# Kernel tuning notes

Measured on AMD Instinct MI355X. Metric: run time of the kernel, lower is better.

## Reference

```python
import jax, jax.numpy as jnp
import numpy as np

NUM_SAMPLE = 80  # hardcoded in the original forward
NUM_ACT = 6
NUM_OPP = 3


def setup_inputs() -> dict:
    key = jax.random.key(0)
    k0, k1, k2 = jax.random.split(key, 3)
    B, D = 4096, 512
    x = jax.random.normal(k0, (B, D), dtype=jnp.float32)
    # orthogonal init with gain 0.01 -> small weights; approximate scale
    W_opp = jax.random.normal(k1, (NUM_OPP, D, NUM_ACT), dtype=jnp.float32) * 0.01
    b_opp = jnp.zeros((NUM_OPP, NUM_ACT), dtype=jnp.float32)
    W = jax.random.normal(k2, (D + NUM_OPP * NUM_ACT, NUM_ACT), dtype=jnp.float32) * 0.01
    b = jnp.zeros((NUM_ACT,), dtype=jnp.float32)
    return {"x": x, "W_opp": W_opp, "b_opp": b_opp, "W": W, "b": b}


def reference(x, W_opp, b_opp, W, b):
    B, D = x.shape
    # --- opponent actors: small linear + softmax, vectorized over the 3 opponents ---
    logits = jnp.einsum('bd,kda->kba', x, W_opp) + b_opp[:, None, :]   # [3,B,6]
    dist = jax.nn.softmax(logits, axis=-1)                              # [3,B,6]
    logp = jax.nn.log_softmax(logits, axis=-1)
    # entropy.mean() per opponent, then sum/3 == mean over opponents
    entropy = (-(dist * logp).sum(-1)).mean(-1).mean()

    # --- vectorized categorical sampling: 80 samples per opponent per batch elem ---
    skey = jax.random.key(42)
    samples = jax.random.categorical(skey, logits[:, None], axis=-1,
                                     shape=(NUM_OPP, NUM_SAMPLE, B))   # [3,S,B] int

    # gather sampled-action probabilities
    probs = jnp.take_along_axis(dist[:, None], samples[..., None], axis=-1)[..., 0]  # [3,S,B]
    probs_bt = jnp.transpose(probs, (0, 2, 1))                          # [3,B,S]
    p1 = probs_bt[0] * probs_bt[1] * probs_bt[2]                        # [B,S]
    p2 = p1 / p1.sum(axis=1, keepdims=True)                             # normalized joint weights

    # actions3[b,s,k] = sampled action of opponent k, sample s, batch b
    acts = jnp.transpose(samples, (2, 1, 0))                            # [B,S,3]
    oh = jax.nn.one_hot(acts, NUM_ACT, dtype=x.dtype).reshape(B, NUM_SAMPLE, NUM_OPP * NUM_ACT)  # [B,S,18]

    xa = jnp.broadcast_to(x[:, None, :], (B, NUM_SAMPLE, D))            # replicate x per sample
    a = jnp.concatenate([xa, oh], axis=2)                               # [B,S,D+18]
    agent_probs = jax.nn.softmax(a @ W + b, axis=-1)                    # [B,S,6]

    actions_probs = jnp.einsum('bs,bsa->ba', p2, agent_probs)           # [B,6]
    return actions_probs, dist, entropy
```

## Files before the change

kernel.cpp:

```cpp
#include <hip/hip_runtime.h>
#include <stdint.h>

#define NUM_ACT 6
#define NUM_OPP 3
#define NUM_SAMPLE 80
#define BATCH 4096
#define DIM 512
#define ACC_STRIDE 98304
#define TROWS 32
#define ENT_IDX 98304

__device__ __forceinline__ uint32_t rotl32(uint32_t x, int d) {
  return (x << d) | (x >> (32 - d));
}

__device__ __forceinline__ void tf_round4(uint32_t& x0, uint32_t& x1,
                                          int r0, int r1, int r2, int r3) {
  x0 += x1; x1 = rotl32(x1, r0); x1 ^= x0;
  x0 += x1; x1 = rotl32(x1, r1); x1 ^= x0;
  x0 += x1; x1 = rotl32(x1, r2); x1 ^= x0;
  x0 += x1; x1 = rotl32(x1, r3); x1 ^= x0;
}

__device__ __forceinline__ void threefry2x32(uint32_t k0, uint32_t k1,
                                             uint32_t& x0, uint32_t& x1) {
  const uint32_t ks2 = k0 ^ k1 ^ 0x1BD11BDAu;
  x0 += k0;  x1 += k1;
  tf_round4(x0, x1, 13, 15, 26, 6);  x0 += k1;  x1 += ks2 + 1u;
  tf_round4(x0, x1, 17, 29, 16, 24); x0 += ks2; x1 += k0  + 2u;
  tf_round4(x0, x1, 13, 15, 26, 6);  x0 += k0;  x1 += k1  + 3u;
  tf_round4(x0, x1, 17, 29, 16, 24); x0 += k1;  x1 += ks2 + 4u;
  tf_round4(x0, x1, 13, 15, 26, 6);  x0 += ks2; x1 += k0  + 5u;
}

__device__ __forceinline__ float jax_uniform(uint32_t flat_idx) {
  uint32_t x0 = 0u, x1 = flat_idx;
  threefry2x32(0u, 42u, x0, x1);
  uint32_t bits = x0 ^ x1;
  return __uint_as_float((bits >> 9) | 0x3f800000u) - 1.0f;
}

__device__ __forceinline__ void dot4(float& a, float4 u, float4 v) {
  a = fmaf(u.x, v.x, a); a = fmaf(u.y, v.y, a);
  a = fmaf(u.z, v.z, a); a = fmaf(u.w, v.w, a);
}

template<int NCH>
__global__ __launch_bounds__(128) void k1_gemm(
    const float* __restrict__ x, const float* __restrict__ Wopp,
    const float* __restrict__ W, float* __restrict__ part,
    float* __restrict__ out) {
  constexpr int WIDTH = 512 / NCH;
  constexpr int XSTR = WIDTH + 4;
  const int tile = blockIdx.x / NCH;
  const int ch = blockIdx.x % NCH;
  const int rowbase = tile * TROWS;
  const int dbase = ch * WIDTH;
  __shared__ float xs[TROWS * XSTR];
  __shared__ float wt[24 * XSTR];
  const int t = threadIdx.x;

  for (int f = t; f < TROWS * (WIDTH / 4); f += 128) {
    int row = f / (WIDTH / 4), c4 = (f % (WIDTH / 4)) << 2;
    float4 v = *(const float4*)(x + (size_t)(rowbase + row) * DIM + dbase + c4);
    *(float4*)(xs + row * XSTR + c4) = v;
  }
  for (int i = t; i < 24 * WIDTH; i += 128) {
    int c = i % 24, dd = i / 24;
    int d = dbase + dd;
    float v = (c < 18) ? Wopp[(c / 6) * (DIM * 6) + d * 6 + (c % 6)]
                       : W[d * 6 + (c - 18)];
    wt[c * XSTR + dd] = v;
  }
  __syncthreads();

  const int rowg = t >> 3, colg = t & 7;
  float acc[2][3] = {{0.f, 0.f, 0.f}, {0.f, 0.f, 0.f}};
  const float* xp = xs + (rowg * 2) * XSTR;
  const float* wp = wt + (colg * 3) * XSTR;
#pragma unroll 4
  for (int dd = 0; dd < WIDTH; dd += 4) {
    float4 x0 = *(const float4*)(xp + dd);
    float4 x1 = *(const float4*)(xp + XSTR + dd);
    float4 w0 = *(const float4*)(wp + dd);
    float4 w1 = *(const float4*)(wp + XSTR + dd);
    float4 w2 = *(const float4*)(wp + 2 * XSTR + dd);
    dot4(acc[0][0], x0, w0); dot4(acc[0][1], x0, w1); dot4(acc[0][2], x0, w2);
    dot4(acc[1][0], x1, w0); dot4(acc[1][1], x1, w1); dot4(acc[1][2], x1, w2);
  }
  const int r0 = rowbase + rowg * 2, c0 = colg * 3;
  float* p = part + (size_t)ch * ACC_STRIDE;
#pragma unroll
  for (int rr = 0; rr < 2; rr++)
#pragma unroll
    for (int cc = 0; cc < 3; cc++)
      p[(r0 + rr) * 24 + c0 + cc] = acc[rr][cc];
  if (blockIdx.x == 0 && t == 0) out[ENT_IDX] = 0.f;
}

#define WSTR 144

template<int NCH>
__global__ __launch_bounds__(1024) void k3f(
    const float* __restrict__ part, const float* __restrict__ bopp,
    const float* __restrict__ W, const float* __restrict__ bias,
    float* __restrict__ out) {
  const int w = threadIdx.x >> 6;
  const int l = threadIdx.x & 63;
  const int b = blockIdx.x * 16 + w;
  __shared__ float lds[16][WSTR];
  __shared__ float s_Hw[16];
  float* L = lds[w];

  if (l < 54) {
    float2 v = *(const float2*)(W + DIM * NUM_ACT + 2 * l);
    L[2 * l] = v.x; L[2 * l + 1] = v.y;
  }

  float colsum = 0.f;
  if (l < 24) {
    float s = (l < 18) ? bopp[l] : bias[l - 18];
#pragma unroll
    for (int g = 0; g < NCH; g++)
      s += part[g * ACC_STRIDE + b * 24 + l];
    colsum = s;
    if (l >= 18) L[136 + (l - 18)] = s;
  }
  const int kk = (l < NUM_OPP) ? l : 0;
  float lg[NUM_ACT];
#pragma unroll
  for (int a = 0; a < NUM_ACT; a++)
    lg[a] = __shfl(colsum, kk * NUM_ACT + a);

  float H = 0.f;
  if (l < NUM_OPP) {
    const int k = l;
    float m = lg[0];
#pragma unroll
    for (int a = 1; a < NUM_ACT; a++) m = fmaxf(m, lg[a]);
    float e[NUM_ACT], Z = 0.f;
#pragma unroll
    for (int a = 0; a < NUM_ACT; a++) { e[a] = expf(lg[a] - m); Z += e[a]; }
    float logZ = logf(Z);
#pragma unroll
    for (int a = 0; a < NUM_ACT; a++) {
      float pa = e[a] / Z;
      L[112 + k * NUM_ACT + a] = pa;
      H -= pa * ((lg[a] - m) - logZ);
    }
  }
  H += __shfl_down(H, 1);
  H += __shfl_down(H, 2);
  if (l == 0) s_Hw[w] = H;

  __syncthreads();
  if (threadIdx.x == 0) {
    float hs = 0.f;
#pragma unroll
    for (int i = 0; i < 16; i++) hs += s_Hw[i];
    atomicAdd(out + ENT_IDX, hs * (1.0f / 12288.0f));
  }

  float d[18];
#pragma unroll
  for (int i = 0; i < 18; i++) d[i] = L[112 + i];

  int   act_a[3];
  float pr_a[3];
#pragma unroll
  for (int k = 0; k < NUM_OPP; k++) {
    float u = jax_uniform((uint32_t)(k * NUM_SAMPLE + l) * BATCH + (uint32_t)b);
    float c = d[k * 6 + 0], pr = d[k * 6 + 0];
    int sel = 0;
#pragma unroll
    for (int a = 1; a < NUM_ACT; a++) {
      bool take = (u >= c);
      sel += take ? 1 : 0;
      pr = take ? d[k * 6 + a] : pr;
      c += d[k * 6 + a];
    }
    act_a[k] = sel; pr_a[k] = pr;
  }
  float prb = 0.f; int actb = 0;
  if (l < 48) {
    const int k = l >> 4, s = 64 + (l & 15);
    float u = jax_uniform((uint32_t)(k * NUM_SAMPLE + s) * BATCH + (uint32_t)b);
    float c = L[112 + k * 6 + 0], pr = c;
    int sel = 0;
#pragma unroll
    for (int a = 1; a < NUM_ACT; a++) {
      float da = L[112 + k * 6 + a];
      bool take = (u >= c);
      sel += take ? 1 : 0;
      pr = take ? da : pr;
      c += da;
    }
    actb = sel; prb = pr;
  }
  const int tm = l & 15;
  float pb0 = __shfl(prb, tm), pb1 = __shfl(prb, tm + 16), pb2 = __shfl(prb, tm + 32);
  int   ab0 = __shfl(actb, tm), ab1 = __shfl(actb, tm + 16), ab2 = __shfl(actb, tm + 32);

  const bool hasb = l < (NUM_SAMPLE - 64);
  float p1a = pr_a[0] * pr_a[1] * pr_a[2];
  float p1b = 0.f;
  if (hasb) p1b = pb0 * pb1 * pb2;
  float tot = p1a + p1b;
#pragma unroll
  for (int m = 32; m > 0; m >>= 1) tot += __shfl_xor(tot, m);

  float xw[NUM_ACT];
#pragma unroll
  for (int a = 0; a < NUM_ACT; a++) xw[a] = L[136 + a];

  float o[NUM_ACT];
#pragma unroll
  for (int a = 0; a < NUM_ACT; a++) o[a] = 0.f;
  {
    int a0 = act_a[0], a1 = act_a[1], a2 = act_a[2];
    float la[NUM_ACT];
#pragma unroll
    for (int a = 0; a < NUM_ACT; a++)
      la[a] = xw[a] + L[a0 * 6 + a] + L[(6 + a1) * 6 + a] + L[(12 + a2) * 6 + a];
    float m = la[0];
#pragma unroll
    for (int a = 1; a < NUM_ACT; a++) m = fmaxf(m, la[a]);
    float e[NUM_ACT], Z = 0.f;
#pragma unroll
    for (int a = 0; a < NUM_ACT; a++) { e[a] = expf(la[a] - m); Z += e[a]; }
    float wz = (p1a / tot) / Z;
#pragma unroll
    for (int a = 0; a < NUM_ACT; a++) o[a] = wz * e[a];
  }
  if (hasb) {
    float la[NUM_ACT];
#pragma unroll
    for (int a = 0; a < NUM_ACT; a++)
      la[a] = xw[a] + L[ab0 * 6 + a] + L[(6 + ab1) * 6 + a] + L[(12 + ab2) * 6 + a];
    float m = la[0];
#pragma unroll
    for (int a = 1; a < NUM_ACT; a++) m = fmaxf(m, la[a]);
    float e[NUM_ACT], Z = 0.f;
#pragma unroll
    for (int a = 0; a < NUM_ACT; a++) { e[a] = expf(la[a] - m); Z += e[a]; }
    float wz = (p1b / tot) / Z;
#pragma unroll
    for (int a = 0; a < NUM_ACT; a++) o[a] += wz * e[a];
  }
#pragma unroll
  for (int m = 32; m > 0; m >>= 1)
#pragma unroll
    for (int a = 0; a < NUM_ACT; a++) o[a] += __shfl_xor(o[a], m);

  if (l == 0) {
#pragma unroll
    for (int a = 0; a < NUM_ACT; a++) out[b * NUM_ACT + a] = o[a];
  }
  if (l < 18) {
    int k = l / 6, a = l - k * 6;
    out[BATCH * NUM_ACT + ((size_t)k * BATCH + b) * NUM_ACT + a] = L[112 + l];
  }
}

extern "C" void kernel_launch(void* const* d_in, const int* in_sizes, int n_in,
                              void* d_out, int out_size, void* d_ws, size_t ws_size,
                              hipStream_t stream) {
  const float* x    = (const float*)d_in[0];
  const float* Wopp = (const float*)d_in[1];
  const float* bopp = (const float*)d_in[2];
  const float* W    = (const float*)d_in[3];
  const float* bias = (const float*)d_in[4];
  float* out = (float*)d_out;
  float* part = (float*)d_ws;

  size_t need8 = (size_t)8 * ACC_STRIDE * sizeof(float);
  if (ws_size >= need8) {
    k1_gemm<8><<<(BATCH / TROWS) * 8, 128, 0, stream>>>(x, Wopp, W, part, out);
    k3f<8><<<BATCH / 16, 1024, 0, stream>>>(part, bopp, W, bias, out);
  } else {
    k1_gemm<4><<<(BATCH / TROWS) * 4, 128, 0, stream>>>(x, Wopp, W, part, out);
    k3f<4><<<BATCH / 16, 1024, 0, stream>>>(part, bopp, W, bias, out);
  }
}
```

Measured before the change: 83.12 us.

## Fuse GEMM and sampling kernels into one block-per-16-rows kernel

Merges the split-K GEMM kernel and the sampling/softmax kernel into a single kernel, where each 1024-thread block computes the logits for 16 rows with an 8-way in-LDS K split and then reduces the partials in shared memory. This removes the global partial-sum workspace round trip and one kernel launch. The trade-off is that every block reloads the full 512x24 transposed weight set into LDS (about 100 KB of shared memory), which limits occupancy to one block per CU and repeats the weight load across 256 blocks. The entropy accumulator is now zeroed with a hipMemsetAsync.

```diff
diff --git a/kernel.cpp b/kernel.cpp
--- a/kernel.cpp
+++ b/kernel.cpp
@@ -6,8 +6,6 @@
 #define NUM_SAMPLE 80
 #define BATCH 4096
 #define DIM 512
-#define ACC_STRIDE 98304
-#define TROWS 32
 #define ENT_IDX 98304
 
 __device__ __forceinline__ uint32_t rotl32(uint32_t x, int d) {
@@ -45,86 +43,68 @@
   a = fmaf(u.z, v.z, a); a = fmaf(u.w, v.w, a);
 }
 
-template<int NCH>
-__global__ __launch_bounds__(128) void k1_gemm(
+#define O_XS   0
+#define O_WT   8704
+#define O_PART 21760
+#define O_W2   24832
+#define O_DIST 24940
+#define O_XW   25228
+#define O_HW   25324
+
+__global__ __launch_bounds__(1024) void k_all(
     const float* __restrict__ x, const float* __restrict__ Wopp,
-    const float* __restrict__ W, float* __restrict__ part,
-    float* __restrict__ out) {
-  constexpr int WIDTH = 512 / NCH;
-  constexpr int XSTR = WIDTH + 4;
-  const int tile = blockIdx.x / NCH;
-  const int ch = blockIdx.x % NCH;
-  const int rowbase = tile * TROWS;
-  const int dbase = ch * WIDTH;
-  __shared__ float xs[TROWS * XSTR];
-  __shared__ float wt[24 * XSTR];
+    const float* __restrict__ bopp, const float* __restrict__ W,
+    const float* __restrict__ bias, float* __restrict__ out) {
+  __shared__ float sm[25340];
   const int t = threadIdx.x;
-
-  for (int f = t; f < TROWS * (WIDTH / 4); f += 128) {
-    int row = f / (WIDTH / 4), c4 = (f % (WIDTH / 4)) << 2;
-    float4 v = *(const float4*)(x + (size_t)(rowbase + row) * DIM + dbase + c4);
-    *(float4*)(xs + row * XSTR + c4) = v;
-  }
-  for (int i = t; i < 24 * WIDTH; i += 128) {
-    int c = i % 24, dd = i / 24;
-    int d = dbase + dd;
+  const int w = t >> 6;
+  const int l = t & 63;
+  const int rowbase = blockIdx.x * 16;
+  const int b = rowbase + w;
+
+  for (int u = t; u < 16 * 128; u += 1024) {
+    int row = u >> 7, c4 = (u & 127) << 2;
+    float4 v = *(const float4*)(x + (size_t)(rowbase + row) * DIM + c4);
+    *(float4*)(sm + O_XS + (c4 >> 6) * 1088 + row * 68 + (c4 & 63)) = v;
+  }
+  for (int i = t; i < 24 * 512; i += 1024) {
+    int d = i / 24, c = i % 24;
     float v = (c < 18) ? Wopp[(c / 6) * (DIM * 6) + d * 6 + (c % 6)]
                        : W[d * 6 + (c - 18)];
-    wt[c * XSTR + dd] = v;
+    sm[O_WT + (d >> 6) * 1632 + c * 68 + (d & 63)] = v;
+  }
+  if (t < 54) {
+    float2 v = *(const float2*)(W + DIM * NUM_ACT + 2 * t);
+    sm[O_W2 + 2 * t] = v.x; sm[O_W2 + 2 * t + 1] = v.y;
   }
   __syncthreads();
 
-  const int rowg = t >> 3, colg = t & 7;
-  float acc[2][3] = {{0.f, 0.f, 0.f}, {0.f, 0.f, 0.f}};
-  const float* xp = xs + (rowg * 2) * XSTR;
-  const float* wp = wt + (colg * 3) * XSTR;
+  {
+    const int sub = t >> 7, tt = t & 127;
+    const int row = tt >> 3, colg = tt & 7;
+    const float* xp = sm + O_XS + sub * 1088 + row * 68;
+    const float* wp = sm + O_WT + sub * 1632 + (colg * 3) * 68;
+    float a0 = 0.f, a1 = 0.f, a2 = 0.f;
 #pragma unroll 4
-  for (int dd = 0; dd < WIDTH; dd += 4) {
-    float4 x0 = *(const float4*)(xp + dd);
-    float4 x1 = *(const float4*)(xp + XSTR + dd);
-    float4 w0 = *(const float4*)(wp + dd);
-    float4 w1 = *(const float4*)(wp + XSTR + dd);
-    float4 w2 = *(const float4*)(wp + 2 * XSTR + dd);
-    dot4(acc[0][0], x0, w0); dot4(acc[0][1], x0, w1); dot4(acc[0][2], x0, w2);
-    dot4(acc[1][0], x1, w0); dot4(acc[1][1], x1, w1); dot4(acc[1][2], x1, w2);
-  }
-  const int r0 = rowbase + rowg * 2, c0 = colg * 3;
-  float* p = part + (size_t)ch * ACC_STRIDE;
-#pragma unroll
-  for (int rr = 0; rr < 2; rr++)
-#pragma unroll
-    for (int cc = 0; cc < 3; cc++)
-      p[(r0 + rr) * 24 + c0 + cc] = acc[rr][cc];
-  if (blockIdx.x == 0 && t == 0) out[ENT_IDX] = 0.f;
-}
-
-#define WSTR 144
-
-template<int NCH>
-__global__ __launch_bounds__(1024) void k3f(
-    const float* __restrict__ part, const float* __restrict__ bopp,
-    const float* __restrict__ W, const float* __restrict__ bias,
-    float* __restrict__ out) {
-  const int w = threadIdx.x >> 6;
-  const int l = threadIdx.x & 63;
-  const int b = blockIdx.x * 16 + w;
-  __shared__ float lds[16][WSTR];
-  __shared__ float s_Hw[16];
-  float* L = lds[w];
-
-  if (l < 54) {
-    float2 v = *(const float2*)(W + DIM * NUM_ACT + 2 * l);
-    L[2 * l] = v.x; L[2 * l + 1] = v.y;
-  }
+    for (int dd = 0; dd < 64; dd += 4) {
+      float4 xv = *(const float4*)(xp + dd);
+      dot4(a0, xv, *(const float4*)(wp + dd));
+      dot4(a1, xv, *(const float4*)(wp + 68 + dd));
+      dot4(a2, xv, *(const float4*)(wp + 136 + dd));
+    }
+    float* pp = sm + O_PART + sub * 384 + row * 24 + colg * 3;
+    pp[0] = a0; pp[1] = a1; pp[2] = a2;
+  }
+  __syncthreads();
 
   float colsum = 0.f;
   if (l < 24) {
     float s = (l < 18) ? bopp[l] : bias[l - 18];
 #pragma unroll
-    for (int g = 0; g < NCH; g++)
-      s += part[g * ACC_STRIDE + b * 24 + l];
+    for (int g = 0; g < 8; g++)
+      s += sm[O_PART + g * 384 + w * 24 + l];
     colsum = s;
-    if (l >= 18) L[136 + (l - 18)] = s;
+    if (l >= 18) sm[O_XW + w * 6 + (l - 18)] = s;
   }
   const int kk = (l < NUM_OPP) ? l : 0;
   float lg[NUM_ACT];
@@ -145,25 +125,25 @@
 #pragma unroll
     for (int a = 0; a < NUM_ACT; a++) {
       float pa = e[a] / Z;
-      L[112 + k * NUM_ACT + a] = pa;
+      sm[O_DIST + w * 18 + k * NUM_ACT + a] = pa;
       H -= pa * ((lg[a] - m) - logZ);
     }
   }
   H += __shfl_down(H, 1);
   H += __shfl_down(H, 2);
-  if (l == 0) s_Hw[w] = H;
+  if (l == 0) sm[O_HW + w] = H;
 
   __syncthreads();
-  if (threadIdx.x == 0) {
+  if (t == 0) {
     float hs = 0.f;
 #pragma unroll
-    for (int i = 0; i < 16; i++) hs += s_Hw[i];
+    for (int i = 0; i < 16; i++) hs += sm[O_HW + i];
     atomicAdd(out + ENT_IDX, hs * (1.0f / 12288.0f));
   }
 
   float d[18];
 #pragma unroll
-  for (int i = 0; i < 18; i++) d[i] = L[112 + i];
+  for (int i = 0; i < 18; i++) d[i] = sm[O_DIST + w * 18 + i];
 
   int   act_a[3];
   float pr_a[3];
@@ -185,11 +165,11 @@
   if (l < 48) {
     const int k = l >> 4, s = 64 + (l & 15);
     float u = jax_uniform((uint32_t)(k * NUM_SAMPLE + s) * BATCH + (uint32_t)b);
-    float c = L[112 + k * 6 + 0], pr = c;
+    float c = sm[O_DIST + w * 18 + k * 6 + 0], pr = c;
     int sel = 0;
 #pragma unroll
     for (int a = 1; a < NUM_ACT; a++) {
-      float da = L[112 + k * 6 + a];
+      float da = sm[O_DIST + w * 18 + k * 6 + a];
       bool take = (u >= c);
       sel += take ? 1 : 0;
       pr = take ? da : pr;
@@ -211,7 +191,7 @@
 
   float xw[NUM_ACT];
 #pragma unroll
-  for (int a = 0; a < NUM_ACT; a++) xw[a] = L[136 + a];
+  for (int a = 0; a < NUM_ACT; a++) xw[a] = sm[O_XW + w * 6 + a];
 
   float o[NUM_ACT];
 #pragma unroll
@@ -221,7 +201,8 @@
     float la[NUM_ACT];
 #pragma unroll
     for (int a = 0; a < NUM_ACT; a++)
-      la[a] = xw[a] + L[a0 * 6 + a] + L[(6 + a1) * 6 + a] + L[(12 + a2) * 6 + a];
+      la[a] = xw[a] + sm[O_W2 + a0 * 6 + a] + sm[O_W2 + (6 + a1) * 6 + a]
+                    + sm[O_W2 + (12 + a2) * 6 + a];
     float m = la[0];
 #pragma unroll
     for (int a = 1; a < NUM_ACT; a++) m = fmaxf(m, la[a]);
@@ -236,7 +217,8 @@
     float la[NUM_ACT];
 #pragma unroll
     for (int a = 0; a < NUM_ACT; a++)
-      la[a] = xw[a] + L[ab0 * 6 + a] + L[(6 + ab1) * 6 + a] + L[(12 + ab2) * 6 + a];
+      la[a] = xw[a] + sm[O_W2 + ab0 * 6 + a] + sm[O_W2 + (6 + ab1) * 6 + a]
+                    + sm[O_W2 + (12 + ab2) * 6 + a];
     float m = la[0];
 #pragma unroll
     for (int a = 1; a < NUM_ACT; a++) m = fmaxf(m, la[a]);
@@ -258,7 +240,8 @@
   }
   if (l < 18) {
     int k = l / 6, a = l - k * 6;
-    out[BATCH * NUM_ACT + ((size_t)k * BATCH + b) * NUM_ACT + a] = L[112 + l];
+    out[BATCH * NUM_ACT + ((size_t)k * BATCH + b) * NUM_ACT + a] =
+        sm[O_DIST + w * 18 + l];
   }
 }
 
@@ -271,14 +254,7 @@
   const float* W    = (const float*)d_in[3];
   const float* bias = (const float*)d_in[4];
   float* out = (float*)d_out;
-  float* part = (float*)d_ws;
-
-  size_t need8 = (size_t)8 * ACC_STRIDE * sizeof(float);
-  if (ws_size >= need8) {
-    k1_gemm<8><<<(BATCH / TROWS) * 8, 128, 0, stream>>>(x, Wopp, W, part, out);
-    k3f<8><<<BATCH / 16, 1024, 0, stream>>>(part, bopp, W, bias, out);
-  } else {
-    k1_gemm<4><<<(BATCH / TROWS) * 4, 128, 0, stream>>>(x, Wopp, W, part, out);
-    k3f<4><<<BATCH / 16, 1024, 0, stream>>>(part, bopp, W, bias, out);
-  }
-}
+
+  hipMemsetAsync(out + ENT_IDX, 0, sizeof(float), stream);
+  k_all<<<BATCH / 16, 1024, 0, stream>>>(x, Wopp, bopp, W, bias, out);
+}
```

Result: faster. 81.42 us (-2.0%).
